# Performance work log

Measured on AMD Instinct MI355X. Metric: run time of the kernel, lower is better.

The kernel has to match this reference:

```python
import jax, jax.numpy as jnp
import numpy as np

T = 100.0  # temperature, from init_kwargs
B = 4096
D = 128
NUM_CLASSES = 10


def setup_inputs() -> dict:
    key = jax.random.key(0)
    kx, ky = jax.random.split(key)
    x = jax.random.normal(kx, (B, D), dtype=jnp.float32)
    y = jax.random.randint(ky, (B,), 0, NUM_CLASSES, dtype=jnp.int64)
    return {"x": x, "y": y}


def reference(x, y):
    # Pairwise squared Euclidean distances: dist[i,j] = ||x_i - x_j||^2
    sq = jnp.sum(x * x, axis=1)                      # [b]
    dist = sq[:, None] + sq[None, :] - 2.0 * (x @ x.T)  # [b, b]
    dist = jnp.maximum(dist, 0.0)                    # clamp fp error; diag -> 0

    e = jnp.exp(-dist / T)                           # [b, b]; e[i,i] = 1

    b = x.shape[0]
    same = (y[:, None] == y[None, :])                # same-label mask
    not_self = ~jnp.eye(b, dtype=bool)

    # numerator: sum over j != i with y[j] == y[i]
    num = jnp.sum(jnp.where(same & not_self, e, 0.0), axis=1)  # [b]
    # denominator: sum over ALL j, including j == i (exp(0) = 1), as in the
    # original loop where the denominator accumulates unconditionally
    den = jnp.sum(e, axis=1)                         # [b]

    return jnp.mean(-jnp.log(num / den))
```

## Files before the change

kernel.cpp:

```cpp
#include <hip/hip_runtime.h>
#include <hip/hip_bf16.h>

#define NB 4096
#define NTB 32

typedef short v8s __attribute__((ext_vector_type(8)));
typedef float v4f __attribute__((ext_vector_type(4)));


__global__ __launch_bounds__(256) void prep_kernel(const float* __restrict__ x,
        float* __restrict__ sq, float* __restrict__ out,
        unsigned short* __restrict__ xb) {
    int tid = threadIdx.x;
    int row = blockIdx.x * 8 + (tid >> 5);
    int lane = tid & 31;
    const float4* xg = (const float4*)x;
    float4 v = xg[row * 32 + lane];
    __hip_bfloat16 h0 = __float2bfloat16(v.x), h1 = __float2bfloat16(v.y);
    __hip_bfloat16 h2 = __float2bfloat16(v.z), h3 = __float2bfloat16(v.w);
    ushort4 u4;
    u4.x = *(unsigned short*)&h0; u4.y = *(unsigned short*)&h1;
    u4.z = *(unsigned short*)&h2; u4.w = *(unsigned short*)&h3;
    ((ushort4*)xb)[row * 32 + lane] = u4;
    float s = v.x * v.x + v.y * v.y + v.z * v.z + v.w * v.w;
    #pragma unroll
    for (int off = 16; off > 0; off >>= 1) s += __shfl_down(s, off);
    if (lane == 0) sq[row] = s;
    if (blockIdx.x == 0 && tid == 0) out[0] = 0.f;
}

__global__ __launch_bounds__(256) void snn_sym(const unsigned short* __restrict__ xb,
        const int* __restrict__ y, const float* __restrict__ sqg,
        float2* __restrict__ P) {
    __shared__ __align__(16) union {
        unsigned short tiles[2 * 128 * 136];
        float part[2 * 128 * 34];
    } sm;
    __shared__ float2 part2[2][128];
    __shared__ float sqi[128], sqj[128];
    __shared__ int yi[128], yj[128];

    const int tid = threadIdx.x;
    const int wave = tid >> 6;
    const int lane = tid & 63;
    const int wm = wave >> 1;
    const int wn = wave & 1;
    const int lr = lane & 15;
    const int q  = lane >> 4;

    int t = blockIdx.x, bi = 0, rem = NTB;
    while (t >= rem) { t -= rem; ++bi; --rem; }
    const int bj = bi + t;
    const int i0 = bi * 128, j0 = bj * 128;
    const bool diag = (bi == bj);

    const v8s* xg = (const v8s*)xb;
    unsigned short* At = sm.tiles;
    unsigned short* Bt = diag ? sm.tiles : sm.tiles + 128 * 136;

    #pragma unroll
    for (int r = 0; r < 8; ++r) {
        int c = r * 256 + tid;
        int row = c >> 4, cc = c & 15;
        *(v8s*)&At[row * 136 + cc * 8] = xg[(i0 + row) * 16 + cc];
        if (!diag)
            *(v8s*)&Bt[row * 136 + cc * 8] = xg[(j0 + row) * 16 + cc];
    }
    if (tid < 128) {
        sqi[tid] = sqg[i0 + tid]; sqj[tid] = sqg[j0 + tid];
        yi[tid] = y[i0 + tid];    yj[tid] = y[j0 + tid];
    }
    __syncthreads();

    v4f acc[4][4];
    #pragma unroll
    for (int mt = 0; mt < 4; ++mt)
        #pragma unroll
        for (int nt = 0; nt < 4; ++nt)
            acc[mt][nt] = (v4f){0.f, 0.f, 0.f, 0.f};

    #pragma unroll
    for (int kk = 0; kk < 4; ++kk) {
        v8s af[4], bf[4];
        #pragma unroll
        for (int mt = 0; mt < 4; ++mt)
            af[mt] = *(const v8s*)&At[(wm * 64 + mt * 16 + lr) * 136 + kk * 32 + q * 8];
        #pragma unroll
        for (int nt = 0; nt < 4; ++nt)
            bf[nt] = *(const v8s*)&Bt[(wn * 64 + nt * 16 + lr) * 136 + kk * 32 + q * 8];
        #pragma unroll
        for (int mt = 0; mt < 4; ++mt)
            #pragma unroll
            for (int nt = 0; nt < 4; ++nt)
                acc[mt][nt] = __builtin_amdgcn_mfma_f32_16x16x32_bf16(
                    af[mt], bf[nt], acc[mt][nt], 0, 0, 0);
    }

    __syncthreads();

    float sqj_r[4]; int yj_r[4], jgl[4];
    #pragma unroll
    for (int nt = 0; nt < 4; ++nt) {
        int jc = wn * 64 + nt * 16 + lr;
        sqj_r[nt] = sqj[jc]; yj_r[nt] = yj[jc]; jgl[nt] = j0 + jc;
    }
    float cn[4] = {0.f, 0.f, 0.f, 0.f}, cd[4] = {0.f, 0.f, 0.f, 0.f};
    #pragma unroll
    for (int mt = 0; mt < 4; ++mt) {
        #pragma unroll
        for (int r = 0; r < 4; ++r) {
            int rloc = wm * 64 + mt * 16 + q * 4 + r;
            float si = sqi[rloc]; int yir = yi[rloc]; int ig = i0 + rloc;
            float n = 0.f, d = 0.f;
            #pragma unroll
            for (int nt = 0; nt < 4; ++nt) {
                float dist = fmaxf(si + sqj_r[nt] - 2.f * acc[mt][nt][r], 0.f);
                float e = __builtin_amdgcn_exp2f(dist * -0.014426950408889634f);
                d += e;
                float me = (yir == yj_r[nt] && ig != jgl[nt]) ? e : 0.f;
                n += me;
                cd[nt] += e; cn[nt] += me;
            }
            *(float2*)&sm.part[((wn * 128 + rloc) * 17 + lr) * 2] = make_float2(n, d);
        }
    }
    #pragma unroll
    for (int nt = 0; nt < 4; ++nt) {
        float n2 = cn[nt] + __shfl_xor(cn[nt], 16); n2 += __shfl_xor(n2, 32);
        float d2 = cd[nt] + __shfl_xor(cd[nt], 16); d2 += __shfl_xor(d2, 32);
        if (q == 0) part2[wm][wn * 64 + nt * 16 + lr] = make_float2(n2, d2);
    }
    __syncthreads();

    {
        int row = tid >> 1, h = tid & 1;
        const float2* p = (const float2*)&sm.part[(h * 128 + row) * 34];
        float sn = 0.f, sd = 0.f;
        #pragma unroll
        for (int c = 0; c < 16; ++c) { float2 v = p[c]; sn += v.x; sd += v.y; }
        sn += __shfl_down(sn, 1); sd += __shfl_down(sd, 1);
        if (h == 0) P[(bi * NTB + bj) * 128 + row] = make_float2(sn, sd);
    }
    if (!diag && tid < 128) {
        float2 a = part2[0][tid], b = part2[1][tid];
        P[(bj * NTB + bi) * 128 + tid] = make_float2(a.x + b.x, a.y + b.y);
    }
}

__global__ __launch_bounds__(256) void snn_final(const float2* __restrict__ P,
        float* __restrict__ out) {
    __shared__ float wsum[4];
    int i = blockIdx.x * 256 + threadIdx.x;
    int ib = i >> 7, il = i & 127;
    float n = 0.f, d = 0.f;
    #pragma unroll
    for (int s = 0; s < NTB; ++s) {
        float2 v = P[(ib * NTB + s) * 128 + il];
        n += v.x; d += v.y;
    }
    float l = -__logf(n / d);
    #pragma unroll
    for (int off = 32; off > 0; off >>= 1) l += __shfl_down(l, off);
    if ((threadIdx.x & 63) == 0) wsum[threadIdx.x >> 6] = l;
    __syncthreads();
    if (threadIdx.x == 0)
        atomicAdd(out, (wsum[0] + wsum[1] + wsum[2] + wsum[3]) * (1.0f / NB));
}

extern "C" void kernel_launch(void* const* d_in, const int* in_sizes, int n_in,
                              void* d_out, int out_size, void* d_ws, size_t ws_size,
                              hipStream_t stream) {
    const float* x = (const float*)d_in[0];
    const int*   y = (const int*)d_in[1];
    float* out = (float*)d_out;
    float* sq  = (float*)d_ws;
    unsigned short* xb = (unsigned short*)(sq + NB);
    float2* P = (float2*)(xb + NB * 128);

    prep_kernel<<<NB / 8, 256, 0, stream>>>(x, sq, out, xb);
    snn_sym<<<NTB * (NTB + 1) / 2, 256, 0, stream>>>(xb, y, sq, P);
    snn_final<<<NB / 256, 256, 0, stream>>>(P, out);
}
```

Baseline: 74.54 us.

## Shrink symmetric tiles to 64 and fuse final reduction via last-block tickets

The pairwise tile size drops from 128 to 64, so the launch grows from 528 to 2080 blocks, giving better CU occupancy on the GPU at the cost of more redundant loads. The separate final kernel is removed. The last 16 blocks to finish take tickets from an atomic counter, spin until every tile is done, then reduce the partial sums and add the loss. This saves one launch but depends on all blocks being co-resident or making forward progress, and it adds a spin-wait.

```diff
diff --git a/kernel.cpp b/kernel.cpp
--- a/kernel.cpp
+++ b/kernel.cpp
@@ -2,14 +2,17 @@
 #include <hip/hip_bf16.h>
 
 #define NB 4096
-#define NTB 32
+#define NT2 64
+#define NOFF 2016
+#define NTILE 2080
+#define NFIN 16
 
 typedef short v8s __attribute__((ext_vector_type(8)));
 typedef float v4f __attribute__((ext_vector_type(4)));
 
 
 __global__ __launch_bounds__(256) void prep_kernel(const float* __restrict__ x,
-        float* __restrict__ sq, float* __restrict__ out,
+        float* __restrict__ sq, float* __restrict__ out, int* __restrict__ cnt,
         unsigned short* __restrict__ xb) {
     int tid = threadIdx.x;
     int row = blockIdx.x * 8 + (tid >> 5);
@@ -26,145 +29,148 @@
     #pragma unroll
     for (int off = 16; off > 0; off >>= 1) s += __shfl_down(s, off);
     if (lane == 0) sq[row] = s;
-    if (blockIdx.x == 0 && tid == 0) out[0] = 0.f;
+    if (blockIdx.x == 0 && tid == 0) { out[0] = 0.f; cnt[0] = 0; }
 }
 
-__global__ __launch_bounds__(256) void snn_sym(const unsigned short* __restrict__ xb,
-        const int* __restrict__ y, const float* __restrict__ sqg,
-        float2* __restrict__ P) {
+__global__ __launch_bounds__(256, 4) void snn64(
+        const unsigned short* __restrict__ xb, const int* __restrict__ y,
+        const float* __restrict__ sqg, float2* __restrict__ Q2,
+        int* __restrict__ cnt, float* __restrict__ out) {
     __shared__ __align__(16) union {
-        unsigned short tiles[2 * 128 * 136];
-        float part[2 * 128 * 34];
+        unsigned short tiles[2 * 64 * 136];
+        float2 part[2][64][17];
     } sm;
-    __shared__ float2 part2[2][128];
-    __shared__ float sqi[128], sqj[128];
-    __shared__ int yi[128], yj[128];
+    __shared__ float2 part2[2][64];
+    __shared__ float sqi[64], sqj[64];
+    __shared__ int yi[64], yj[64];
+    __shared__ int ticket_s;
+    __shared__ float wsum[4];
 
     const int tid = threadIdx.x;
     const int wave = tid >> 6;
     const int lane = tid & 63;
-    const int wm = wave >> 1;
-    const int wn = wave & 1;
-    const int lr = lane & 15;
-    const int q  = lane >> 4;
+    const int wm = wave >> 1, wn = wave & 1;
+    const int lr = lane & 15, q = lane >> 4;
 
-    int t = blockIdx.x, bi = 0, rem = NTB;
-    while (t >= rem) { t -= rem; ++bi; --rem; }
-    const int bj = bi + t;
-    const int i0 = bi * 128, j0 = bj * 128;
+    int k = blockIdx.x, bi, bj;
+    if (k >= NOFF) { bi = k - NOFF; bj = bi; }
+    else {
+        int tt = k, rem = 63; bi = 0;
+        while (tt >= rem) { tt -= rem; ++bi; --rem; }
+        bj = bi + 1 + tt;
+    }
+    const int i0 = bi * 64, j0 = bj * 64;
     const bool diag = (bi == bj);
+    unsigned short* At = sm.tiles;
+    unsigned short* Bt = diag ? At : At + 64 * 136;
 
     const v8s* xg = (const v8s*)xb;
-    unsigned short* At = sm.tiles;
-    unsigned short* Bt = diag ? sm.tiles : sm.tiles + 128 * 136;
-
     #pragma unroll
-    for (int r = 0; r < 8; ++r) {
+    for (int r = 0; r < 4; ++r) {
         int c = r * 256 + tid;
         int row = c >> 4, cc = c & 15;
         *(v8s*)&At[row * 136 + cc * 8] = xg[(i0 + row) * 16 + cc];
         if (!diag)
             *(v8s*)&Bt[row * 136 + cc * 8] = xg[(j0 + row) * 16 + cc];
     }
-    if (tid < 128) {
-        sqi[tid] = sqg[i0 + tid]; sqj[tid] = sqg[j0 + tid];
-        yi[tid] = y[i0 + tid];    yj[tid] = y[j0 + tid];
+    if (tid < 64) {
+        sqi[tid] = sqg[i0 + tid]; yi[tid] = y[i0 + tid];
+        sqj[tid] = sqg[j0 + tid]; yj[tid] = y[j0 + tid];
     }
     __syncthreads();
 
-    v4f acc[4][4];
+    v4f acc[2][2];
     #pragma unroll
-    for (int mt = 0; mt < 4; ++mt)
+    for (int mt = 0; mt < 2; ++mt)
         #pragma unroll
-        for (int nt = 0; nt < 4; ++nt)
+        for (int nt = 0; nt < 2; ++nt)
             acc[mt][nt] = (v4f){0.f, 0.f, 0.f, 0.f};
-
     #pragma unroll
     for (int kk = 0; kk < 4; ++kk) {
-        v8s af[4], bf[4];
-        #pragma unroll
-        for (int mt = 0; mt < 4; ++mt)
-            af[mt] = *(const v8s*)&At[(wm * 64 + mt * 16 + lr) * 136 + kk * 32 + q * 8];
-        #pragma unroll
-        for (int nt = 0; nt < 4; ++nt)
-            bf[nt] = *(const v8s*)&Bt[(wn * 64 + nt * 16 + lr) * 136 + kk * 32 + q * 8];
-        #pragma unroll
-        for (int mt = 0; mt < 4; ++mt)
-            #pragma unroll
-            for (int nt = 0; nt < 4; ++nt)
-                acc[mt][nt] = __builtin_amdgcn_mfma_f32_16x16x32_bf16(
-                    af[mt], bf[nt], acc[mt][nt], 0, 0, 0);
+        v8s a0 = *(const v8s*)&At[(wm * 32 + lr) * 136 + kk * 32 + q * 8];
+        v8s a1 = *(const v8s*)&At[(wm * 32 + 16 + lr) * 136 + kk * 32 + q * 8];
+        v8s b0 = *(const v8s*)&Bt[(wn * 32 + lr) * 136 + kk * 32 + q * 8];
+        v8s b1 = *(const v8s*)&Bt[(wn * 32 + 16 + lr) * 136 + kk * 32 + q * 8];
+        acc[0][0] = __builtin_amdgcn_mfma_f32_16x16x32_bf16(a0, b0, acc[0][0], 0, 0, 0);
+        acc[0][1] = __builtin_amdgcn_mfma_f32_16x16x32_bf16(a0, b1, acc[0][1], 0, 0, 0);
+        acc[1][0] = __builtin_amdgcn_mfma_f32_16x16x32_bf16(a1, b0, acc[1][0], 0, 0, 0);
+        acc[1][1] = __builtin_amdgcn_mfma_f32_16x16x32_bf16(a1, b1, acc[1][1], 0, 0, 0);
     }
-
     __syncthreads();
 
-    float sqj_r[4]; int yj_r[4], jgl[4];
+    float sqj_r[2]; int yj_r[2], jgl[2];
     #pragma unroll
-    for (int nt = 0; nt < 4; ++nt) {
-        int jc = wn * 64 + nt * 16 + lr;
+    for (int nt = 0; nt < 2; ++nt) {
+        int jc = wn * 32 + nt * 16 + lr;
         sqj_r[nt] = sqj[jc]; yj_r[nt] = yj[jc]; jgl[nt] = j0 + jc;
     }
-    float cn[4] = {0.f, 0.f, 0.f, 0.f}, cd[4] = {0.f, 0.f, 0.f, 0.f};
+    float cn[2] = {0.f, 0.f}, cd[2] = {0.f, 0.f};
     #pragma unroll
-    for (int mt = 0; mt < 4; ++mt) {
+    for (int mt = 0; mt < 2; ++mt)
         #pragma unroll
         for (int r = 0; r < 4; ++r) {
-            int rloc = wm * 64 + mt * 16 + q * 4 + r;
+            int rloc = wm * 32 + mt * 16 + q * 4 + r;
             float si = sqi[rloc]; int yir = yi[rloc]; int ig = i0 + rloc;
             float n = 0.f, d = 0.f;
             #pragma unroll
-            for (int nt = 0; nt < 4; ++nt) {
+            for (int nt = 0; nt < 2; ++nt) {
                 float dist = fmaxf(si + sqj_r[nt] - 2.f * acc[mt][nt][r], 0.f);
                 float e = __builtin_amdgcn_exp2f(dist * -0.014426950408889634f);
-                d += e;
                 float me = (yir == yj_r[nt] && ig != jgl[nt]) ? e : 0.f;
-                n += me;
+                d += e; n += me;
                 cd[nt] += e; cn[nt] += me;
             }
-            *(float2*)&sm.part[((wn * 128 + rloc) * 17 + lr) * 2] = make_float2(n, d);
+            sm.part[wn][rloc][lr] = make_float2(n, d);
         }
-    }
     #pragma unroll
-    for (int nt = 0; nt < 4; ++nt) {
+    for (int nt = 0; nt < 2; ++nt) {
         float n2 = cn[nt] + __shfl_xor(cn[nt], 16); n2 += __shfl_xor(n2, 32);
         float d2 = cd[nt] + __shfl_xor(cd[nt], 16); d2 += __shfl_xor(d2, 32);
-        if (q == 0) part2[wm][wn * 64 + nt * 16 + lr] = make_float2(n2, d2);
+        if (q == 0) part2[wm][wn * 32 + nt * 16 + lr] = make_float2(n2, d2);
     }
     __syncthreads();
 
-    {
+    if (tid < 128) {
         int row = tid >> 1, h = tid & 1;
-        const float2* p = (const float2*)&sm.part[(h * 128 + row) * 34];
         float sn = 0.f, sd = 0.f;
         #pragma unroll
-        for (int c = 0; c < 16; ++c) { float2 v = p[c]; sn += v.x; sd += v.y; }
+        for (int c = 0; c < 16; ++c) {
+            float2 v = sm.part[h][row][c]; sn += v.x; sd += v.y;
+        }
         sn += __shfl_down(sn, 1); sd += __shfl_down(sd, 1);
-        if (h == 0) P[(bi * NTB + bj) * 128 + row] = make_float2(sn, sd);
+        if (h == 0) Q2[bj * NB + i0 + row] = make_float2(sn, sd);
     }
-    if (!diag && tid < 128) {
+    if (!diag && tid < 64) {
         float2 a = part2[0][tid], b = part2[1][tid];
-        P[(bj * NTB + bi) * 128 + tid] = make_float2(a.x + b.x, a.y + b.y);
+        Q2[bi * NB + j0 + tid] = make_float2(a.x + b.x, a.y + b.y);
     }
-}
 
-__global__ __launch_bounds__(256) void snn_final(const float2* __restrict__ P,
-        float* __restrict__ out) {
-    __shared__ float wsum[4];
-    int i = blockIdx.x * 256 + threadIdx.x;
-    int ib = i >> 7, il = i & 127;
-    float n = 0.f, d = 0.f;
-    #pragma unroll
-    for (int s = 0; s < NTB; ++s) {
-        float2 v = P[(ib * NTB + s) * 128 + il];
-        n += v.x; d += v.y;
+    __threadfence();
+    if (tid == 0) ticket_s = atomicAdd(cnt, 1);
+    __syncthreads();
+    if (ticket_s >= NTILE - NFIN) {
+        if (tid == 0) {
+            while (__hip_atomic_load(cnt, __ATOMIC_RELAXED,
+                                     __HIP_MEMORY_SCOPE_AGENT) < NTILE)
+                __builtin_amdgcn_s_sleep(2);
+        }
+        __syncthreads();
+        __threadfence();
+        int i = (ticket_s - (NTILE - NFIN)) * 256 + tid;
+        float n = 0.f, d = 0.f;
+        #pragma unroll 8
+        for (int b = 0; b < NT2; ++b) {
+            float2 v = Q2[b * NB + i];
+            n += v.x; d += v.y;
+        }
+        float l = -__logf(n / d);
+        #pragma unroll
+        for (int off = 32; off > 0; off >>= 1) l += __shfl_down(l, off);
+        if (lane == 0) wsum[wave] = l;
+        __syncthreads();
+        if (tid == 0)
+            atomicAdd(out, (wsum[0] + wsum[1] + wsum[2] + wsum[3]) * (1.0f / NB));
     }
-    float l = -__logf(n / d);
-    #pragma unroll
-    for (int off = 32; off > 0; off >>= 1) l += __shfl_down(l, off);
-    if ((threadIdx.x & 63) == 0) wsum[threadIdx.x >> 6] = l;
-    __syncthreads();
-    if (threadIdx.x == 0)
-        atomicAdd(out, (wsum[0] + wsum[1] + wsum[2] + wsum[3]) * (1.0f / NB));
 }
 
 extern "C" void kernel_launch(void* const* d_in, const int* in_sizes, int n_in,
@@ -174,10 +180,10 @@
     const int*   y = (const int*)d_in[1];
     float* out = (float*)d_out;
     float* sq  = (float*)d_ws;
-    unsigned short* xb = (unsigned short*)(sq + NB);
-    float2* P = (float2*)(xb + NB * 128);
+    int*   cnt = (int*)(sq + NB);
+    unsigned short* xb = (unsigned short*)(sq + NB + 16);
+    float2* Q2 = (float2*)(xb + NB * 128);
 
-    prep_kernel<<<NB / 8, 256, 0, stream>>>(x, sq, out, xb);
-    snn_sym<<<NTB * (NTB + 1) / 2, 256, 0, stream>>>(xb, y, sq, P);
-    snn_final<<<NB / 256, 256, 0, stream>>>(P, out);
+    prep_kernel<<<NB / 8, 256, 0, stream>>>(x, sq, out, cnt, xb);
+    snn64<<<NTILE, 256, 0, stream>>>(xb, y, sq, Q2, cnt, out);
 }
```

Measured after the change: 212.3 us. 185% more time.
